# Performance work log

Measured on AMD Instinct MI355X. Metric: run time of the kernel, lower is better.

Reference implementation:

```python
import jax, jax.numpy as jnp
import numpy as np

B = 4096
HASH_BITS = 128
TEACHER_DIM = 768
TEMPERATURE = 0.2
CONTRASTIVE_W = 1.0
DISTILL_W = 0.5
QUANT_W = 0.01


def _l2_normalize(x, eps=1e-12):
    # matches torch F.normalize(dim=-1)
    n = jnp.sqrt(jnp.sum(x * x, axis=-1, keepdims=True))
    return x / jnp.maximum(n, eps)


def setup_inputs() -> dict:
    key = jax.random.key(0)
    k1, k2, k3, k4 = jax.random.split(key, 4)
    logits = jax.random.normal(k1, (B, HASH_BITS), dtype=jnp.float32)
    # binary {-1,+1} codes as in the module contract
    hash_codes = jnp.sign(jax.random.normal(k2, (B, HASH_BITS), dtype=jnp.float32))
    hash_codes = jnp.where(hash_codes == 0, 1.0, hash_codes)
    teacher_embed = jax.random.normal(k3, (B, TEACHER_DIM), dtype=jnp.float32)
    # sparse random positives plus self-positives (guarantees each row nonempty)
    rand_pos = jax.random.uniform(k4, (B, B)) < 0.002
    eye = jnp.eye(B, dtype=bool)
    positive_mask = rand_pos | eye
    return {
        "logits": logits,
        "hash_codes": hash_codes,
        "teacher_embed": teacher_embed,
        "positive_mask": positive_mask,
    }


def reference(logits, hash_codes, teacher_embed, positive_mask):
    teacher = _l2_normalize(teacher_embed)

    # ---- contrastive (vectorized form of the per-row python loop) ----
    ln = _l2_normalize(logits)
    sim = (ln @ ln.T) / TEMPERATURE  # [B, B]
    eye = jnp.eye(sim.shape[0], dtype=bool)
    sim_masked = jnp.where(eye, -jnp.inf, sim)
    # per-row stable logsumexp over self-masked similarities
    log_denom = jax.nn.logsumexp(sim_masked, axis=1)  # [B]
    pm = positive_mask.astype(sim.dtype)
    cnt = pm.sum(axis=1)  # [B]
    pos_mean = (sim * pm).sum(axis=1) / jnp.maximum(cnt, 1.0)
    has_pos = cnt > 0
    per_row = jnp.where(has_pos, -pos_mean + log_denom, 0.0)
    num_pos = jnp.maximum(has_pos.sum(), 1)
    loss_cont = per_row.sum() / num_pos.astype(sim.dtype)

    # ---- distillation: hash similarity vs teacher similarity MSE ----
    hash_sim = (hash_codes @ hash_codes.T) / hash_codes.shape[-1]
    teacher_sim = teacher @ teacher.T
    loss_distill = jnp.mean((hash_sim - teacher_sim) ** 2)

    # ---- quantization: push |logits| toward 1 ----
    loss_quant = jnp.mean(jnp.abs(jnp.abs(logits) - 1.0))

    total = (
        CONTRASTIVE_W * loss_cont
        + DISTILL_W * loss_distill
        + QUANT_W * loss_quant
    )
    return total
```

## Files before the change

### kernel.cpp

```cpp
#include <hip/hip_runtime.h>


typedef __bf16 bf16x8 __attribute__((ext_vector_type(8)));
typedef float f32x4 __attribute__((ext_vector_type(4)));

__device__ __forceinline__ unsigned short f2bf(float f) {
  union { float f; unsigned int u; } v; v.f = f;
  unsigned int u = v.u;
  return (unsigned short)((u + 0x7FFFu + ((u >> 16) & 1u)) >> 16);
}

__device__ __forceinline__ void atomAddF(float* p, float v) {
  unsafeAtomicAdd(p, v);
}

__global__ __launch_bounds__(256) void prep(const float* __restrict__ logits,
                                            const float* __restrict__ hash,
                                            const float* __restrict__ teacher,
                                            unsigned short* __restrict__ P,
                                            unsigned char* __restrict__ QT,
                                            float* __restrict__ qpart,
                                            float* __restrict__ rowexp,
                                            float* __restrict__ possum,
                                            float* __restrict__ cntw,
                                            float* __restrict__ dtot) {
  __shared__ float rnt[16];
  __shared__ unsigned char QL[16 * 897];
  const int t = threadIdx.x, wave = t >> 6, lane = t & 63;
  const int r0 = (int)blockIdx.x * 16;

#pragma unroll
  for (int rr = 0; rr < 4; ++rr) {
    const int rl = wave * 4 + rr, r = r0 + rl;
    float ss = 0.f;
#pragma unroll
    for (int i = 0; i < 3; ++i) {
      const float4 v = *(const float4*)&teacher[(size_t)r * 768 + i * 256 + lane * 4];
      ss += v.x * v.x + v.y * v.y + v.z * v.z + v.w * v.w;
    }
    const float2 lv = *(const float2*)&logits[(size_t)r * 128 + lane * 2];
    float ssl = lv.x * lv.x + lv.y * lv.y;
    float qv = fabsf(fabsf(lv.x) - 1.f) + fabsf(fabsf(lv.y) - 1.f);
#pragma unroll
    for (int off = 1; off < 64; off <<= 1) {
      ss += __shfl_xor(ss, off, 64);
      ssl += __shfl_xor(ssl, off, 64);
      qv += __shfl_xor(qv, off, 64);
    }
    const float rnl = 1.f / fmaxf(sqrtf(ssl), 1e-12f);
    const unsigned int pk = (unsigned int)f2bf(lv.x * rnl) |
                            ((unsigned int)f2bf(lv.y * rnl) << 16);
    *(unsigned int*)&P[(size_t)r * 128 + lane * 2] = pk;
    if (lane == 0) {
      rnt[rl] = 11.313708498984761f / fmaxf(sqrtf(ss), 1e-12f);
      qpart[r] = qv;
    }
  }
  if (t < 16) { rowexp[r0 + t] = 0.f; possum[r0 + t] = 0.f; cntw[r0 + t] = 0.f; }
  if (blockIdx.x == 0 && t == 0) *dtot = 0.f;
  __syncthreads();

#pragma unroll
  for (int it = 0; it < 4; ++it) {
    const int task = it * 256 + t;
    if (task < 896) {
      const int r = task / 56, cb = task % 56;
      const int r_g = r0 + r;
      unsigned char* dst = &QL[r * 897 + cb * 16];
      if (cb < 8) {
        const float4 v0 = *(const float4*)&hash[(size_t)r_g * 128 + cb * 16];
        const float4 v1 = *(const float4*)&hash[(size_t)r_g * 128 + cb * 16 + 4];
        const float4 v2 = *(const float4*)&hash[(size_t)r_g * 128 + cb * 16 + 8];
        const float4 v3 = *(const float4*)&hash[(size_t)r_g * 128 + cb * 16 + 12];
        const float vv[16] = {v0.x, v0.y, v0.z, v0.w, v1.x, v1.y, v1.z, v1.w,
                              v2.x, v2.y, v2.z, v2.w, v3.x, v3.y, v3.z, v3.w};
#pragma unroll
        for (int k = 0; k < 16; ++k) dst[k] = vv[k] >= 0.f ? 0x38 : 0xB8;
      } else {
        const float sc = rnt[r];
        const int c0 = cb * 16 - 128;
        const float4 v0 = *(const float4*)&teacher[(size_t)r_g * 768 + c0];
        const float4 v1 = *(const float4*)&teacher[(size_t)r_g * 768 + c0 + 4];
        const float4 v2 = *(const float4*)&teacher[(size_t)r_g * 768 + c0 + 8];
        const float4 v3 = *(const float4*)&teacher[(size_t)r_g * 768 + c0 + 12];
        const float vv[16] = {v0.x, v0.y, v0.z, v0.w, v1.x, v1.y, v1.z, v1.w,
                              v2.x, v2.y, v2.z, v2.w, v3.x, v3.y, v3.z, v3.w};
#pragma unroll
        for (int k = 0; k < 16; ++k) {
          const int p8 = __builtin_amdgcn_cvt_pk_fp8_f32(vv[k] * sc, vv[k] * sc,
                                                         0, false);
          dst[k] = (unsigned char)(p8 & 0xFF);
        }
      }
    }
  }
  __syncthreads();

#pragma unroll
  for (int i = 0; i < 4; ++i) {
    const int c = t + 256 * i;
    if (c < 896) {
      unsigned char buf[16];
#pragma unroll
      for (int j = 0; j < 16; ++j) buf[j] = QL[j * 897 + c];
      *(uint4*)&QT[(size_t)c * 4096 + r0] = *(uint4*)buf;
    }
  }
}

#define STAGE_GEN(GA, GB, PITCH, BASE)                                         \
  {                                                                            \
    _Pragma("unroll") for (int it = 0; it < 4; ++it) {                         \
      const int task = it * 256 + t;                                           \
      const int row = task >> 3;                                               \
      const int c16 = (task & 7) ^ (row & 7);                                  \
      const unsigned char* gpA = (GA) + (size_t)row * (PITCH) + c16 * 16;      \
      __builtin_amdgcn_global_load_lds(                                        \
          (const __attribute__((address_space(1))) void*)gpA,                  \
          (__attribute__((address_space(3))) void*)                            \
              &SB[(BASE) + it * 4096 + wave * 1024],                           \
          16, 0, 0);                                                           \
      if (offdiag) {                                                           \
        const unsigned char* gpB = (GB) + (size_t)row * (PITCH) + c16 * 16;    \
        __builtin_amdgcn_global_load_lds(                                      \
            (const __attribute__((address_space(1))) void*)gpB,                \
            (__attribute__((address_space(3))) void*)                         \
                &SB[(BASE) + 16384 + it * 4096 + wave * 1024],                 \
            16, 0, 0);                                                         \
      }                                                                        \
    }                                                                          \
  }

#define MFMA_B(BASE)                                                           \
  {                                                                            \
    _Pragma("unroll") for (int ks = 0; ks < 2; ++ks) {                         \
      const int ph = ((ks * 4 + qd) ^ (l15 & 7)) * 16;                         \
      bf16x8 af[4], bfr[4];                                                    \
      _Pragma("unroll") for (int rt = 0; rt < 4; ++rt)                         \
          af[rt] = *(const bf16x8*)&SB[(BASE) +                                \
                                       (wy * 64 + rt * 16 + l15) * 128 + ph];  \
      _Pragma("unroll") for (int ct = 0; ct < 4; ++ct)                         \
          bfr[ct] = *(const bf16x8*)&SB[(BASE) + boffB +                       \
                                        (wx * 64 + ct * 16 + l15) * 128 + ph]; \
      _Pragma("unroll") for (int rt = 0; rt < 4; ++rt)                         \
          _Pragma("unroll") for (int ct = 0; ct < 4; ++ct) acc[rt][ct] =       \
          __builtin_amdgcn_mfma_f32_16x16x32_bf16(af[rt], bfr[ct],             \
                                                  acc[rt][ct], 0, 0, 0);       \
    }                                                                          \
  }

#define MFMA_Q(BASE)                                                           \
  {                                                                            \
    _Pragma("unroll") for (int ks = 0; ks < 4; ++ks) {                         \
      const int g0 = ks * 4 + qd;                                              \
      const int ph = ((g0 >> 1) ^ (l15 & 7)) * 16 + (g0 & 1) * 8;              \
      long af[4], bfr[4];                                                      \
      _Pragma("unroll") for (int rt = 0; rt < 4; ++rt)                         \
          af[rt] = *(const long*)&SB[(BASE) +                                  \
                                     (wy * 64 + rt * 16 + l15) * 128 + ph];    \
      _Pragma("unroll") for (int ct = 0; ct < 4; ++ct)                         \
          bfr[ct] = *(const long*)&SB[(BASE) + boffB +                         \
                                      (wx * 64 + ct * 16 + l15) * 128 + ph];   \
      _Pragma("unroll") for (int rt = 0; rt < 4; ++rt)                         \
          _Pragma("unroll") for (int ct = 0; ct < 4; ++ct) acc[rt][ct] =       \
          __builtin_amdgcn_mfma_f32_16x16x32_fp8_fp8(af[rt], bfr[ct],          \
                                                     acc[rt][ct], 0, 0, 0);    \
    }                                                                          \
  }

__global__ __launch_bounds__(256, 2) void mega(const unsigned short* __restrict__ P,
                                               const unsigned char* __restrict__ QT,
                                               const void* __restrict__ mask,
                                               float* __restrict__ rowexp,
                                               float* __restrict__ possum,
                                               float* __restrict__ cntw,
                                               float* __restrict__ Cpart) {
  __shared__ __align__(16) unsigned char SB[65536];
  __shared__ float redrow[128][2];

  const int t = threadIdx.x;
  const int wave = t >> 6, lane = t & 63;
  const int qd = lane >> 4, l15 = lane & 15;
  const int wy = wave >> 1, wx = wave & 1;
  const int b = (int)blockIdx.x;

  f32x4 acc[4][4];
#pragma unroll
  for (int rt = 0; rt < 4; ++rt)
#pragma unroll
    for (int ct = 0; ct < 4; ++ct) acc[rt][ct] = {0.f, 0.f, 0.f, 0.f};

  if (b < 112) {
    const int tile = b >> 2, ksl = b & 3;
    int I = 0, rem = tile;
    while (rem >= 7 - I) { rem -= 7 - I; ++I; }
    const int J = I + rem;
    const bool offdiag = (I != J);
    const int boffB = offdiag ? 16384 : 0;
    const unsigned char* QA = QT + (size_t)I * 128 * 4096 + ksl * 1024;
    const unsigned char* QB = QT + (size_t)J * 128 * 4096 + ksl * 1024;

    STAGE_GEN(QA, QB, 4096, 0);
    __syncthreads();
    for (int kc = 0; kc < 8; ++kc) {
      const int cb = (kc & 1) * 32768;
      if (kc < 7) STAGE_GEN(QA + (kc + 1) * 128, QB + (kc + 1) * 128, 4096,
                            cb ^ 32768);
      MFMA_Q(cb);
      __syncthreads();
    }
    float* Ct = Cpart + ((size_t)(tile * 4 + ksl)) * 16384 + t * 64;
#pragma unroll
    for (int rt = 0; rt < 4; ++rt)
#pragma unroll
      for (int ct = 0; ct < 4; ++ct)
        *(f32x4*)&Ct[(rt * 4 + ct) * 4] = acc[rt][ct];
  } else {
    const int bb = b - 112;
    const int l = (bb & 7) * 128 + (bb >> 3);
    const int bi = l >> 5, bj = l & 31;
    const int ti = bi * 128, tj = bj * 128;
    const bool offdiag = (bi != bj);
    const int boffB = offdiag ? 16384 : 0;
    const bool is_byte = ((const unsigned char*)mask)[4097] != 0;

    const unsigned char* Pa = (const unsigned char*)(P + (size_t)ti * 128);
    const unsigned char* Pb = (const unsigned char*)(P + (size_t)tj * 128);

    STAGE_GEN(Pa, Pb, 256, 0);
    __syncthreads();
    STAGE_GEN(Pa + 128, Pb + 128, 256, 32768);
    MFMA_B(0);
    __syncthreads();
    if (is_byte) {
      const unsigned char* m8d = (const unsigned char*)mask + (size_t)ti * 4096 + tj;
#pragma unroll
      for (int it = 0; it < 4; ++it) {
        const int task = it * 256 + t;
        const int row = task >> 3, seg = task & 7;
        __builtin_amdgcn_global_load_lds(
            (const __attribute__((address_space(1))) void*)
                (m8d + (size_t)row * 4096 + seg * 16),
            (__attribute__((address_space(3))) void*)&SB[it * 4096 + wave * 1024],
            16, 0, 0);
      }
    }
    MFMA_B(32768);
    __syncthreads();
    if (!is_byte) {
      const unsigned int* m32 = (const unsigned int*)mask;
#pragma unroll
      for (int it = 0; it < 16; ++it) {
        const int task = it * 256 + t;
        const int row = task >> 5, seg = task & 31;
        const uint4 v = *(const uint4*)&m32[(size_t)(ti + row) * 4096 + tj + seg * 4];
        uchar4 pk;
        pk.x = v.x ? 1 : 0; pk.y = v.y ? 1 : 0;
        pk.z = v.z ? 1 : 0; pk.w = v.w ? 1 : 0;
        *(uchar4*)&SB[row * 128 + seg * 4] = pk;
      }
      __syncthreads();
    }

#pragma unroll
    for (int rt = 0; rt < 4; ++rt) {
#pragma unroll
      for (int r = 0; r < 4; ++r) {
        const int mrow = wy * 64 + rt * 16 + qd * 4 + r;
        const int m = ti + mrow;
        float se = 0.f;
#pragma unroll
        for (int ct = 0; ct < 4; ++ct) {
          const int ncol = wx * 64 + ct * 16 + l15;
          const int n = tj + ncol;
          const float sim = acc[rt][ct][r] * 5.0f;
          const float e = __expf(sim);
          if (m != n) se += e;
          if (SB[mrow * 128 + ncol]) {
            atomAddF(&possum[m], sim);
            atomAddF(&cntw[m], 1.0f);
          }
        }
#pragma unroll
        for (int off = 1; off < 16; off <<= 1) se += __shfl_xor(se, off, 64);
        if (l15 == 0) redrow[mrow][wx] = se;
      }
    }
    __syncthreads();
    if (t < 128) atomAddF(&rowexp[ti + t], redrow[t][0] + redrow[t][1]);
  }
}

__global__ __launch_bounds__(256) void gsq(const float* __restrict__ Cpart,
                                           float* __restrict__ dtot) {
  const int t = threadIdx.x;
  const int wave = t >> 6, lane = t & 63;
  float s = 0.f;
  for (int e = (int)blockIdx.x * 256 + t; e < 458752; e += 448 * 256) {
    const int tile = e >> 14, idx = e & 16383;
    int I = 0, rem = tile;
    while (rem >= 7 - I) { rem -= 7 - I; ++I; }
    const int J = I + rem;
    float v = 0.f;
#pragma unroll
    for (int k = 0; k < 4; ++k)
      v += Cpart[((size_t)(tile * 4 + k)) * 16384 + idx];
    const float w = (I == J ? 1.f : 2.f) * (((I == 0) == (J == 0)) ? 1.f : -1.f);
    s += w * v * v;
  }
#pragma unroll
  for (int off = 1; off < 64; off <<= 1) s += __shfl_xor(s, off, 64);
  __shared__ float sw[4];
  if (lane == 0) sw[wave] = s;
  __syncthreads();
  if (t == 0) atomAddF(dtot, sw[0] + sw[1] + sw[2] + sw[3]);
}

__global__ __launch_bounds__(1024) void finalize(const float* __restrict__ rowexp,
                                                 const float* __restrict__ possum,
                                                 const float* __restrict__ cnt,
                                                 const float* __restrict__ qpart,
                                                 const float* __restrict__ dtot,
                                                 float* __restrict__ out) {
  const int t = threadIdx.x;
  const int wave = t >> 6, lane = t & 63;
  float c = 0.f, q = 0.f;
  for (int m = t; m < 4096; m += 1024) {
    c += logf(rowexp[m]) - possum[m] / fmaxf(cnt[m], 1.0f);
    q += qpart[m];
  }
#pragma unroll
  for (int off = 1; off < 64; off <<= 1) {
    c += __shfl_xor(c, off, 64);
    q += __shfl_xor(q, off, 64);
  }
  __shared__ float sc[16], sq[16];
  if (lane == 0) { sc[wave] = c; sq[wave] = q; }
  __syncthreads();
  if (t == 0) {
    float C = 0.f, Q = 0.f;
    for (int i = 0; i < 16; ++i) { C += sc[i]; Q += sq[i]; }
    out[0] = C * (1.0f / 4096.0f) + 0.5f * (dtot[0] * 3.6379788e-12f) +
             0.01f * (Q * (1.0f / 524288.0f));
  }
}

extern "C" void kernel_launch(void* const* d_in, const int* in_sizes, int n_in,
                              void* d_out, int out_size, void* d_ws, size_t ws_size,
                              hipStream_t stream) {
  const float* logits = (const float*)d_in[0];
  const float* hash = (const float*)d_in[1];
  const float* teacher = (const float*)d_in[2];
  const void* mask = d_in[3];
  float* out = (float*)d_out;

  char* ws = (char*)d_ws;
  float* rowexp = (float*)(ws + 0);
  float* possum = (float*)(ws + 16384);
  float* cntw = (float*)(ws + 32768);
  float* qpart = (float*)(ws + 49152);
  float* dtot = (float*)(ws + 65536);
  unsigned short* P = (unsigned short*)(ws + 98304);
  unsigned char* QT = (unsigned char*)(ws + 98304 + 1048576);
  float* Cpart = (float*)(ws + 98304 + 1048576 + 3670016);

  prep<<<256, 256, 0, stream>>>(logits, hash, teacher, P, QT, qpart, rowexp,
                                possum, cntw, dtot);
  mega<<<1136, 256, 0, stream>>>(P, QT, mask, rowexp, possum, cntw, Cpart);
  gsq<<<448, 256, 0, stream>>>(Cpart, dtot);
  finalize<<<1, 1024, 0, stream>>>(rowexp, possum, cntw, qpart, dtot, out);
}
```

Baseline: 156.5 us.

## Halve mega kernel LDS to single buffer and raise occupancy to four blocks

Shared memory in the mega kernel shrinks from a 64 KB double buffer to a 32 KB single buffer, and launch bounds rise so four blocks can be resident per CU. Staging is now serialized with a sync before and after each MFMA step instead of prefetching the next chunk, so the code relies on extra resident blocks to hide load latency. The exp and row-sum reduction is moved ahead of the mask pass so it overlaps the async mask load. The tighter register budget from the higher launch bound may cause spills, and losing in-block prefetch may expose memory latency.

```diff
diff --git a/kernel.cpp b/kernel.cpp
--- a/kernel.cpp
+++ b/kernel.cpp
@@ -108,7 +108,7 @@
   }
 }
 
-#define STAGE_GEN(GA, GB, PITCH, BASE)                                         \
+#define STAGE_GEN(GA, GB, PITCH)                                               \
   {                                                                            \
     _Pragma("unroll") for (int it = 0; it < 4; ++it) {                         \
       const int task = it * 256 + t;                                           \
@@ -118,29 +118,28 @@
       __builtin_amdgcn_global_load_lds(                                        \
           (const __attribute__((address_space(1))) void*)gpA,                  \
           (__attribute__((address_space(3))) void*)                            \
-              &SB[(BASE) + it * 4096 + wave * 1024],                           \
+              &SB[it * 4096 + wave * 1024],                                    \
           16, 0, 0);                                                           \
       if (offdiag) {                                                           \
         const unsigned char* gpB = (GB) + (size_t)row * (PITCH) + c16 * 16;    \
         __builtin_amdgcn_global_load_lds(                                      \
             (const __attribute__((address_space(1))) void*)gpB,                \
             (__attribute__((address_space(3))) void*)                         \
-                &SB[(BASE) + 16384 + it * 4096 + wave * 1024],                 \
+                &SB[16384 + it * 4096 + wave * 1024],                          \
             16, 0, 0);                                                         \
       }                                                                        \
     }                                                                          \
   }
 
-#define MFMA_B(BASE)                                                           \
+#define MFMA_B()                                                               \
   {                                                                            \
     _Pragma("unroll") for (int ks = 0; ks < 2; ++ks) {                         \
       const int ph = ((ks * 4 + qd) ^ (l15 & 7)) * 16;                         \
       bf16x8 af[4], bfr[4];                                                    \
       _Pragma("unroll") for (int rt = 0; rt < 4; ++rt)                         \
-          af[rt] = *(const bf16x8*)&SB[(BASE) +                                \
-                                       (wy * 64 + rt * 16 + l15) * 128 + ph];  \
+          af[rt] = *(const bf16x8*)&SB[(wy * 64 + rt * 16 + l15) * 128 + ph];  \
       _Pragma("unroll") for (int ct = 0; ct < 4; ++ct)                         \
-          bfr[ct] = *(const bf16x8*)&SB[(BASE) + boffB +                       \
+          bfr[ct] = *(const bf16x8*)&SB[boffB +                                \
                                         (wx * 64 + ct * 16 + l15) * 128 + ph]; \
       _Pragma("unroll") for (int rt = 0; rt < 4; ++rt)                         \
           _Pragma("unroll") for (int ct = 0; ct < 4; ++ct) acc[rt][ct] =       \
@@ -149,17 +148,16 @@
     }                                                                          \
   }
 
-#define MFMA_Q(BASE)                                                           \
+#define MFMA_Q()                                                               \
   {                                                                            \
     _Pragma("unroll") for (int ks = 0; ks < 4; ++ks) {                         \
       const int g0 = ks * 4 + qd;                                              \
       const int ph = ((g0 >> 1) ^ (l15 & 7)) * 16 + (g0 & 1) * 8;              \
       long af[4], bfr[4];                                                      \
       _Pragma("unroll") for (int rt = 0; rt < 4; ++rt)                         \
-          af[rt] = *(const long*)&SB[(BASE) +                                  \
-                                     (wy * 64 + rt * 16 + l15) * 128 + ph];    \
+          af[rt] = *(const long*)&SB[(wy * 64 + rt * 16 + l15) * 128 + ph];    \
       _Pragma("unroll") for (int ct = 0; ct < 4; ++ct)                         \
-          bfr[ct] = *(const long*)&SB[(BASE) + boffB +                         \
+          bfr[ct] = *(const long*)&SB[boffB +                                  \
                                       (wx * 64 + ct * 16 + l15) * 128 + ph];   \
       _Pragma("unroll") for (int rt = 0; rt < 4; ++rt)                         \
           _Pragma("unroll") for (int ct = 0; ct < 4; ++ct) acc[rt][ct] =       \
@@ -168,14 +166,14 @@
     }                                                                          \
   }
 
-__global__ __launch_bounds__(256, 2) void mega(const unsigned short* __restrict__ P,
+__global__ __launch_bounds__(256, 4) void mega(const unsigned short* __restrict__ P,
                                                const unsigned char* __restrict__ QT,
                                                const void* __restrict__ mask,
                                                float* __restrict__ rowexp,
                                                float* __restrict__ possum,
                                                float* __restrict__ cntw,
                                                float* __restrict__ Cpart) {
-  __shared__ __align__(16) unsigned char SB[65536];
+  __shared__ __align__(16) unsigned char SB[32768];
   __shared__ float redrow[128][2];
 
   const int t = threadIdx.x;
@@ -200,13 +198,10 @@
     const unsigned char* QA = QT + (size_t)I * 128 * 4096 + ksl * 1024;
     const unsigned char* QB = QT + (size_t)J * 128 * 4096 + ksl * 1024;
 
-    STAGE_GEN(QA, QB, 4096, 0);
-    __syncthreads();
     for (int kc = 0; kc < 8; ++kc) {
-      const int cb = (kc & 1) * 32768;
-      if (kc < 7) STAGE_GEN(QA + (kc + 1) * 128, QB + (kc + 1) * 128, 4096,
-                            cb ^ 32768);
-      MFMA_Q(cb);
+      STAGE_GEN(QA + kc * 128, QB + kc * 128, 4096);
+      __syncthreads();
+      MFMA_Q();
       __syncthreads();
     }
     float* Ct = Cpart + ((size_t)(tile * 4 + ksl)) * 16384 + t * 64;
@@ -227,11 +222,15 @@
     const unsigned char* Pa = (const unsigned char*)(P + (size_t)ti * 128);
     const unsigned char* Pb = (const unsigned char*)(P + (size_t)tj * 128);
 
-    STAGE_GEN(Pa, Pb, 256, 0);
-    __syncthreads();
-    STAGE_GEN(Pa + 128, Pb + 128, 256, 32768);
-    MFMA_B(0);
-    __syncthreads();
+    STAGE_GEN(Pa, Pb, 256);
+    __syncthreads();
+    MFMA_B();
+    __syncthreads();
+    STAGE_GEN(Pa + 128, Pb + 128, 256);
+    __syncthreads();
+    MFMA_B();
+    __syncthreads();
+
     if (is_byte) {
       const unsigned char* m8d = (const unsigned char*)mask + (size_t)ti * 4096 + tj;
 #pragma unroll
@@ -245,8 +244,32 @@
             16, 0, 0);
       }
     }
-    MFMA_B(32768);
-    __syncthreads();
+
+#pragma unroll
+    for (int rt = 0; rt < 4; ++rt)
+#pragma unroll
+      for (int ct = 0; ct < 4; ++ct) acc[rt][ct] *= 5.0f;
+
+#pragma unroll
+    for (int rt = 0; rt < 4; ++rt) {
+#pragma unroll
+      for (int r = 0; r < 4; ++r) {
+        const int mrow = wy * 64 + rt * 16 + qd * 4 + r;
+        const int m = ti + mrow;
+        float se = 0.f;
+#pragma unroll
+        for (int ct = 0; ct < 4; ++ct) {
+          const int n = tj + wx * 64 + ct * 16 + l15;
+          const float e = __expf(acc[rt][ct][r]);
+          if (m != n) se += e;
+        }
+#pragma unroll
+        for (int off = 1; off < 16; off <<= 1) se += __shfl_xor(se, off, 64);
+        if (l15 == 0) redrow[mrow][wx] = se;
+      }
+    }
+    __syncthreads();
+
     if (!is_byte) {
       const unsigned int* m32 = (const unsigned int*)mask;
 #pragma unroll
@@ -262,32 +285,24 @@
       __syncthreads();
     }
 
+    if (t < 128) atomAddF(&rowexp[ti + t], redrow[t][0] + redrow[t][1]);
+
 #pragma unroll
     for (int rt = 0; rt < 4; ++rt) {
 #pragma unroll
       for (int r = 0; r < 4; ++r) {
         const int mrow = wy * 64 + rt * 16 + qd * 4 + r;
         const int m = ti + mrow;
-        float se = 0.f;
 #pragma unroll
         for (int ct = 0; ct < 4; ++ct) {
           const int ncol = wx * 64 + ct * 16 + l15;
-          const int n = tj + ncol;
-          const float sim = acc[rt][ct][r] * 5.0f;
-          const float e = __expf(sim);
-          if (m != n) se += e;
           if (SB[mrow * 128 + ncol]) {
-            atomAddF(&possum[m], sim);
+            atomAddF(&possum[m], acc[rt][ct][r]);
             atomAddF(&cntw[m], 1.0f);
           }
         }
-#pragma unroll
-        for (int off = 1; off < 16; off <<= 1) se += __shfl_xor(se, off, 64);
-        if (l15 == 0) redrow[mrow][wx] = se;
-      }
-    }
-    __syncthreads();
-    if (t < 128) atomAddF(&rowexp[ti + t], redrow[t][0] + redrow[t][1]);
+      }
+    }
   }
 }
 
```

After: 159.9 us. 2.1% more time.

## Accumulate split-K Gram partials atomically and merge final reduction kernels

Applied to the files above, without the earlier changes.

The mega kernel no longer writes four separate split-K partial tiles of the Gram matrix. It now atomically adds its accumulators into one zeroed buffer, so the squared-sum pass reads a quarter of the data. The gsq and finalize kernels are merged into one 64-block reduce kernel that uses a last-block-done counter to write the output, removing a launch. prep now runs on 8 rows per block with twice as many blocks and also zeroes the buffer. The cost is many float atomics in mega, with contention among the four k-slices, and nondeterministic summation order.

```diff
diff --git a/kernel.cpp b/kernel.cpp
--- a/kernel.cpp
+++ b/kernel.cpp
@@ -23,15 +23,23 @@
                                             float* __restrict__ rowexp,
                                             float* __restrict__ possum,
                                             float* __restrict__ cntw,
-                                            float* __restrict__ dtot) {
-  __shared__ float rnt[16];
-  __shared__ unsigned char QL[16 * 897];
+                                            float* __restrict__ accs,
+                                            float* __restrict__ Cbuf) {
+  __shared__ float rnt[8];
+  __shared__ unsigned char QL[8 * 897];
   const int t = threadIdx.x, wave = t >> 6, lane = t & 63;
-  const int r0 = (int)blockIdx.x * 16;
-
-#pragma unroll
-  for (int rr = 0; rr < 4; ++rr) {
-    const int rl = wave * 4 + rr, r = r0 + rl;
+  const int r0 = (int)blockIdx.x * 8;
+
+  for (int i = t; i < 224; i += 256)
+    *(f32x4*)&Cbuf[((size_t)blockIdx.x * 224 + i) * 4] = (f32x4){0.f, 0.f, 0.f, 0.f};
+  if (blockIdx.x == 0) {
+    if (t < 4) accs[t] = 0.f;
+    if (t == 4) *(int*)&accs[4] = 0;
+  }
+
+#pragma unroll
+  for (int rr = 0; rr < 2; ++rr) {
+    const int rl = wave * 2 + rr, r = r0 + rl;
     float ss = 0.f;
 #pragma unroll
     for (int i = 0; i < 3; ++i) {
@@ -56,14 +64,13 @@
       qpart[r] = qv;
     }
   }
-  if (t < 16) { rowexp[r0 + t] = 0.f; possum[r0 + t] = 0.f; cntw[r0 + t] = 0.f; }
-  if (blockIdx.x == 0 && t == 0) *dtot = 0.f;
+  if (t < 8) { rowexp[r0 + t] = 0.f; possum[r0 + t] = 0.f; cntw[r0 + t] = 0.f; }
   __syncthreads();
 
 #pragma unroll
-  for (int it = 0; it < 4; ++it) {
+  for (int it = 0; it < 2; ++it) {
     const int task = it * 256 + t;
-    if (task < 896) {
+    if (task < 448) {
       const int r = task / 56, cb = task % 56;
       const int r_g = r0 + r;
       unsigned char* dst = &QL[r * 897 + cb * 16];
@@ -100,10 +107,10 @@
   for (int i = 0; i < 4; ++i) {
     const int c = t + 256 * i;
     if (c < 896) {
-      unsigned char buf[16];
-#pragma unroll
-      for (int j = 0; j < 16; ++j) buf[j] = QL[j * 897 + c];
-      *(uint4*)&QT[(size_t)c * 4096 + r0] = *(uint4*)buf;
+      unsigned char buf[8];
+#pragma unroll
+      for (int j = 0; j < 8; ++j) buf[j] = QL[j * 897 + c];
+      *(uint2*)&QT[(size_t)c * 4096 + r0] = *(uint2*)buf;
     }
   }
 }
@@ -174,7 +181,7 @@
                                                float* __restrict__ rowexp,
                                                float* __restrict__ possum,
                                                float* __restrict__ cntw,
-                                               float* __restrict__ Cpart) {
+                                               float* __restrict__ Cbuf) {
   __shared__ __align__(16) unsigned char SB[65536];
   __shared__ float redrow[128][2];
 
@@ -209,12 +216,14 @@
       MFMA_Q(cb);
       __syncthreads();
     }
-    float* Ct = Cpart + ((size_t)(tile * 4 + ksl)) * 16384 + t * 64;
+    float* Ct = Cbuf + (size_t)tile * 16384;
 #pragma unroll
     for (int rt = 0; rt < 4; ++rt)
 #pragma unroll
       for (int ct = 0; ct < 4; ++ct)
-        *(f32x4*)&Ct[(rt * 4 + ct) * 4] = acc[rt][ct];
+#pragma unroll
+        for (int i = 0; i < 4; ++i)
+          atomAddF(&Ct[(rt * 4 + ct) * 1024 + i * 256 + t], acc[rt][ct][i]);
   } else {
     const int bb = b - 112;
     const int l = (bb & 7) * 128 + (bb >> 3);
@@ -291,57 +300,56 @@
   }
 }
 
-__global__ __launch_bounds__(256) void gsq(const float* __restrict__ Cpart,
-                                           float* __restrict__ dtot) {
+__global__ __launch_bounds__(256) void reduce(const float* __restrict__ rowexp,
+                                              const float* __restrict__ possum,
+                                              const float* __restrict__ cnt,
+                                              const float* __restrict__ qpart,
+                                              const float* __restrict__ Cbuf,
+                                              float* __restrict__ accs,
+                                              float* __restrict__ out) {
   const int t = threadIdx.x;
   const int wave = t >> 6, lane = t & 63;
-  float s = 0.f;
-  for (int e = (int)blockIdx.x * 256 + t; e < 458752; e += 448 * 256) {
-    const int tile = e >> 14, idx = e & 16383;
+  const int g = (int)blockIdx.x * 256 + t;
+
+  float c = 0.f, q = 0.f, d = 0.f;
+  if (g < 4096) {
+    c = logf(rowexp[g]) - possum[g] / fmaxf(cnt[g], 1.0f);
+    q = qpart[g];
+  }
+#pragma unroll
+  for (int k = 0; k < 7; ++k) {
+    const int e4 = g + k * 16384;
+    const int tile = e4 >> 12;
     int I = 0, rem = tile;
     while (rem >= 7 - I) { rem -= 7 - I; ++I; }
     const int J = I + rem;
-    float v = 0.f;
-#pragma unroll
-    for (int k = 0; k < 4; ++k)
-      v += Cpart[((size_t)(tile * 4 + k)) * 16384 + idx];
     const float w = (I == J ? 1.f : 2.f) * (((I == 0) == (J == 0)) ? 1.f : -1.f);
-    s += w * v * v;
-  }
-#pragma unroll
-  for (int off = 1; off < 64; off <<= 1) s += __shfl_xor(s, off, 64);
-  __shared__ float sw[4];
-  if (lane == 0) sw[wave] = s;
-  __syncthreads();
-  if (t == 0) atomAddF(dtot, sw[0] + sw[1] + sw[2] + sw[3]);
-}
-
-__global__ __launch_bounds__(1024) void finalize(const float* __restrict__ rowexp,
-                                                 const float* __restrict__ possum,
-                                                 const float* __restrict__ cnt,
-                                                 const float* __restrict__ qpart,
-                                                 const float* __restrict__ dtot,
-                                                 float* __restrict__ out) {
-  const int t = threadIdx.x;
-  const int wave = t >> 6, lane = t & 63;
-  float c = 0.f, q = 0.f;
-  for (int m = t; m < 4096; m += 1024) {
-    c += logf(rowexp[m]) - possum[m] / fmaxf(cnt[m], 1.0f);
-    q += qpart[m];
+    const f32x4 v = *(const f32x4*)&Cbuf[(size_t)e4 * 4];
+    d += w * (v[0] * v[0] + v[1] * v[1] + v[2] * v[2] + v[3] * v[3]);
   }
 #pragma unroll
   for (int off = 1; off < 64; off <<= 1) {
     c += __shfl_xor(c, off, 64);
     q += __shfl_xor(q, off, 64);
-  }
-  __shared__ float sc[16], sq[16];
-  if (lane == 0) { sc[wave] = c; sq[wave] = q; }
+    d += __shfl_xor(d, off, 64);
+  }
+  __shared__ float sc[4], sq[4], sd[4];
+  if (lane == 0) { sc[wave] = c; sq[wave] = q; sd[wave] = d; }
   __syncthreads();
   if (t == 0) {
-    float C = 0.f, Q = 0.f;
-    for (int i = 0; i < 16; ++i) { C += sc[i]; Q += sq[i]; }
-    out[0] = C * (1.0f / 4096.0f) + 0.5f * (dtot[0] * 3.6379788e-12f) +
-             0.01f * (Q * (1.0f / 524288.0f));
+    atomAddF(&accs[0], sc[0] + sc[1] + sc[2] + sc[3]);
+    atomAddF(&accs[1], sq[0] + sq[1] + sq[2] + sq[3]);
+    atomAddF(&accs[2], sd[0] + sd[1] + sd[2] + sd[3]);
+    __threadfence();
+    const int old = atomicAdd((int*)&accs[4], 1);
+    if (old == 63) {
+      __threadfence();
+      const float C = unsafeAtomicAdd(&accs[0], 0.f);
+      const float Q = unsafeAtomicAdd(&accs[1], 0.f);
+      const float D = unsafeAtomicAdd(&accs[2], 0.f);
+      out[0] = C * (1.0f / 4096.0f) + 0.5f * (D * 3.6379788e-12f) +
+               0.01f * (Q * (1.0f / 524288.0f));
+    }
   }
 }
 
@@ -359,14 +367,13 @@
   float* possum = (float*)(ws + 16384);
   float* cntw = (float*)(ws + 32768);
   float* qpart = (float*)(ws + 49152);
-  float* dtot = (float*)(ws + 65536);
+  float* accs = (float*)(ws + 65536);
   unsigned short* P = (unsigned short*)(ws + 98304);
   unsigned char* QT = (unsigned char*)(ws + 98304 + 1048576);
-  float* Cpart = (float*)(ws + 98304 + 1048576 + 3670016);
-
-  prep<<<256, 256, 0, stream>>>(logits, hash, teacher, P, QT, qpart, rowexp,
-                                possum, cntw, dtot);
-  mega<<<1136, 256, 0, stream>>>(P, QT, mask, rowexp, possum, cntw, Cpart);
-  gsq<<<448, 256, 0, stream>>>(Cpart, dtot);
-  finalize<<<1, 1024, 0, stream>>>(rowexp, possum, cntw, qpart, dtot, out);
-}
+  float* Cbuf = (float*)(ws + 98304 + 1048576 + 3670016);
+
+  prep<<<512, 256, 0, stream>>>(logits, hash, teacher, P, QT, qpart, rowexp,
+                                possum, cntw, accs, Cbuf);
+  mega<<<1136, 256, 0, stream>>>(P, QT, mask, rowexp, possum, cntw, Cbuf);
+  reduce<<<64, 256, 0, stream>>>(rowexp, possum, cntw, qpart, Cbuf, accs, out);
+}
```

Measured after the change: 151.9 us. -3.0%, faster.
